# Performance work log

Measured on AMD Instinct MI355X. Metric: run time of the kernel, lower is better.

Reference implementation:

```python
import jax, jax.numpy as jnp
import numpy as np

N_USER, N_ITEM, D, K, E = 80000, 40000, 128, 10, 2000000

def _mlp(x, w1, b1, w2, b2, w3, b3):
    # MLP from source: linear->tanh->linear->tanh->linear->L2 normalize (eval mode, dropout off)
    x = jnp.tanh(x @ w1 + b1)
    x = jnp.tanh(x @ w2 + b2)
    x = x @ w3 + b3
    return x / jnp.maximum(jnp.linalg.norm(x, axis=-1, keepdims=True), 1e-12)

def setup_inputs() -> dict:
    key = jax.random.key(0)
    ks = jax.random.split(key, 24)
    s = 0.05
    inp = {
        'uemb_s': jax.random.normal(ks[0], (N_USER, D), jnp.float32),
        'iemb_s': jax.random.normal(ks[1], (N_ITEM, D), jnp.float32),
        'uemb_t': jax.random.normal(ks[2], (N_USER, D), jnp.float32),
        'u_emb_sp': jax.random.normal(ks[3], (N_USER, D), jnp.float32),
        'edge_user': jax.random.randint(ks[4], (E,), 0, N_USER, jnp.int32),
        'edge_item': jax.random.randint(ks[5], (E,), 0, N_ITEM, jnp.int32),
        # meta nets
        'Wu': jax.random.normal(ks[6], (4 * D, D), jnp.float32) * s,
        'bu': jnp.zeros((D,), jnp.float32),
        'Wi': jax.random.normal(ks[7], (2 * D, D), jnp.float32) * s,
        'bi': jnp.zeros((D,), jnp.float32),
        # mlp1: D -> D*K -> D//2 -> D*K
        'm1w1': jax.random.normal(ks[8], (D, D * K), jnp.float32) * s,
        'm1b1': jnp.zeros((D * K,), jnp.float32),
        'm1w2': jax.random.normal(ks[9], (D * K, D // 2), jnp.float32) * s,
        'm1b2': jnp.zeros((D // 2,), jnp.float32),
        'm1w3': jax.random.normal(ks[10], (D // 2, D * K), jnp.float32) * s,
        'm1b3': jnp.zeros((D * K,), jnp.float32),
        # mlp2: D -> D*K -> D//2 -> D*K
        'm2w1': jax.random.normal(ks[11], (D, D * K), jnp.float32) * s,
        'm2b1': jnp.zeros((D * K,), jnp.float32),
        'm2w2': jax.random.normal(ks[12], (D * K, D // 2), jnp.float32) * s,
        'm2b2': jnp.zeros((D // 2,), jnp.float32),
        'm2w3': jax.random.normal(ks[13], (D // 2, D * K), jnp.float32) * s,
        'm2b3': jnp.zeros((D * K,), jnp.float32),
    }
    return inp

def reference(uemb_s, iemb_s, uemb_t, u_emb_sp, edge_user, edge_item,
              Wu, bu, Wi, bi,
              m1w1, m1b1, m1w2, m1b2, m1w3, m1b3,
              m2w1, m2b1, m2w2, m2b2, m2w3, m2b3):
    # spmm with all-ones values == gather + segment_sum over the bipartite edge list
    neighbors_u = jax.ops.segment_sum(iemb_s[edge_item], edge_user, num_segments=N_USER)  # [U, D]
    tmp_embu = jax.lax.stop_gradient(
        jnp.concatenate([uemb_s, uemb_t, u_emb_sp, neighbors_u], axis=1)) @ Wu + bu       # [U, D]
    neighbors_i = jax.ops.segment_sum(((uemb_s + u_emb_sp) * 0.5)[edge_user], edge_item,
                                      num_segments=N_ITEM)                               # [I, D]
    tmp_embi = jax.lax.stop_gradient(
        jnp.concatenate([iemb_s, neighbors_i], axis=1)) @ Wi + bi                         # [I, D]
    metau = _mlp(tmp_embu, m1w1, m1b1, m1w2, m1b2, m1w3, m1b3).reshape(-1, D, K)          # [U, D, K]
    metai = _mlp(tmp_embi, m2w1, m2b1, m2w2, m2b2, m2w3, m2b3).reshape(-1, K, D)          # [I, K, D]
    meta_biasu = jnp.mean(metau, axis=0)  # [D, K]
    meta_biasi = jnp.mean(metai, axis=0)  # [K, D]
    low_weightu = jax.nn.softmax(metau + meta_biasu, axis=1)
    low_weighti = jax.nn.softmax(metai + meta_biasi, axis=1)
    return (low_weightu, low_weighti)
```

## Files before the change

### kernel.cpp

```cpp
#include <hip/hip_runtime.h>
#include <hip/hip_bf16.h>

#define D_ 128
#define DK_ 1280
#define K_ 10

typedef __attribute__((ext_vector_type(8))) short bh8;
typedef __attribute__((ext_vector_type(4))) short bh4;
typedef __attribute__((ext_vector_type(4))) float f32x4;

__device__ __forceinline__ short f2b(float f) {
    unsigned u = __builtin_bit_cast(unsigned, f);
    u += 0x7fffu + ((u >> 16) & 1u);
    return (short)(u >> 16);
}
__device__ __forceinline__ float b2f(short s) {
    unsigned u = ((unsigned)(unsigned short)s) << 16;
    return __builtin_bit_cast(float, u);
}
__device__ __forceinline__ float tanh_fast(float x) {
    float e = __expf(2.f * x);
    return 1.f - __fdividef(2.f, e + 1.f);
}
__device__ __forceinline__ f32x4 mfma16(bh8 a, bh8 b, f32x4 c) {
    return __builtin_amdgcn_mfma_f32_16x16x32_bf16(a, b, c, 0, 0, 0);
}

__device__ __forceinline__ int blk_excl_scan(int v, int t) {
    __shared__ int wp[4];
    int lane = t & 63, w = t >> 6;
    int s = v;
    for (int o = 1; o < 64; o <<= 1) {
        int pv = __shfl_up(s, o);
        if (lane >= o) s += pv;
    }
    if (lane == 63) wp[w] = s;
    __syncthreads();
    if (t == 0) {
        int a = 0;
#pragma unroll
        for (int k = 0; k < 4; ++k) { int x = wp[k]; wp[k] = a; a += x; }
    }
    __syncthreads();
    int r = s - v + wp[w];
    __syncthreads();
    return r;
}

__global__ __launch_bounds__(256) void cvt_all(
    const float* __restrict__ us, const float* __restrict__ ut,
    const float* __restrict__ usp, const float* __restrict__ is_,
    short* __restrict__ usb, short* __restrict__ utb,
    short* __restrict__ uspb, short* __restrict__ uavg, short* __restrict__ isb,
    int n4u, int n4i)
{
    int i = blockIdx.x * 256 + threadIdx.x;
    if (i < n4u) {
        float4 a = ((const float4*)us)[i];
        float4 b = ((const float4*)ut)[i];
        float4 c = ((const float4*)usp)[i];
        bh4 sa, sb, sc, sv;
        sa[0] = f2b(a.x); sa[1] = f2b(a.y); sa[2] = f2b(a.z); sa[3] = f2b(a.w);
        sb[0] = f2b(b.x); sb[1] = f2b(b.y); sb[2] = f2b(b.z); sb[3] = f2b(b.w);
        sc[0] = f2b(c.x); sc[1] = f2b(c.y); sc[2] = f2b(c.z); sc[3] = f2b(c.w);
        sv[0] = f2b(0.5f * (a.x + c.x)); sv[1] = f2b(0.5f * (a.y + c.y));
        sv[2] = f2b(0.5f * (a.z + c.z)); sv[3] = f2b(0.5f * (a.w + c.w));
        ((bh4*)usb)[i] = sa; ((bh4*)utb)[i] = sb;
        ((bh4*)uspb)[i] = sc; ((bh4*)uavg)[i] = sv;
    } else if (i < n4u + n4i) {
        int j = i - n4u;
        float4 v = ((const float4*)is_)[j];
        bh4 s;
        s[0] = f2b(v.x); s[1] = f2b(v.y); s[2] = f2b(v.z); s[3] = f2b(v.w);
        ((bh4*)isb)[j] = s;
    }
}

struct PackArgs {
    const float* W[8];
    short* o[8];
    int K[8];
    int N[8];
};
__global__ __launch_bounds__(256) void pack_all(PackArgs pa)
{
    int seg = blockIdx.y;
    int K = pa.K[seg], N = pa.N[seg];
    int total = K * N;
    int o = blockIdx.x * 256 + threadIdx.x;
    if (o >= total) return;
    const float* W = pa.W[seg];
    short* out = pa.o[seg];
    int j    = o & 7;
    int lane = (o >> 3) & 63;
    int rest = o >> 9;
    int KK = K >> 5;
    int kk = rest % KK;
    int tile = rest / KK;
    int k = kk * 32 + (lane >> 4) * 8 + j;
    int n = tile * 16 + (lane & 15);
    out[o] = f2b(W[(size_t)k * N + n]);
}

__global__ __launch_bounds__(256) void bhist_kernel(
    const int* __restrict__ eu, const int* __restrict__ ei,
    int* __restrict__ bcu, int* __restrict__ bci,
    int E, int shu, int shi, int nbu, int nbi)
{
    __shared__ int hu[160], hi[160];
    int t = threadIdx.x;
    int base = blockIdx.x * 4096;
    if (t < 160) { hu[t] = 0; hi[t] = 0; }
    __syncthreads();
    int n = min(4096, E - base);
#pragma unroll 4
    for (int k = 0; k < 16; ++k) {
        int idx = k * 256 + t;
        if (idx < n) {
            atomicAdd(&hu[eu[base + idx] >> shu], 1);
            atomicAdd(&hi[ei[base + idx] >> shi], 1);
        }
    }
    __syncthreads();
    if (t < nbu && hu[t]) atomicAdd(&bcu[t], hu[t]);
    if (t < nbi && hi[t]) atomicAdd(&bci[t], hi[t]);
}

__global__ __launch_bounds__(256) void binit_kernel(
    const int* __restrict__ bcu, int* __restrict__ gcu, int* __restrict__ bbu, int nbu,
    const int* __restrict__ bci, int* __restrict__ gci, int* __restrict__ bbi, int nbi,
    int E)
{
    int t = threadIdx.x;
    {
        int v = (t < nbu) ? bcu[t] : 0;
        int ex = blk_excl_scan(v, t);
        if (t < nbu) { gcu[t] = ex; bbu[t] = ex; }
        if (t == 0) bbu[nbu] = E;
    }
    __syncthreads();
    {
        int v = (t < nbi) ? bci[t] : 0;
        int ex = blk_excl_scan(v, t);
        if (t < nbi) { gci[t] = ex; bbi[t] = ex; }
        if (t == 0) bbi[nbi] = E;
    }
}

__global__ __launch_bounds__(256) void partition_kernel(
    const int* __restrict__ eu, const int* __restrict__ ei,
    int* __restrict__ gcu, int* __restrict__ gci,
    uint2* __restrict__ ebu, uint2* __restrict__ ebi,
    int E, int shu, int shi, int nbu, int nbi)
{
    __shared__ int hu[160], hi[160];
    int t = threadIdx.x;
    int base = blockIdx.x * 4096;
    if (t < 160) { hu[t] = 0; hi[t] = 0; }
    __syncthreads();
    int n = min(4096, E - base);
    int us[16], is_[16];
#pragma unroll 4
    for (int k = 0; k < 16; ++k) {
        int idx = k * 256 + t;
        if (idx < n) {
            us[k] = eu[base + idx];
            is_[k] = ei[base + idx];
            atomicAdd(&hu[us[k] >> shu], 1);
            atomicAdd(&hi[is_[k] >> shi], 1);
        } else us[k] = -1;
    }
    __syncthreads();
    if (t < nbu) { int c = hu[t]; hu[t] = c ? atomicAdd(&gcu[t], c) : 0; }
    if (t < nbi) { int c = hi[t]; hi[t] = c ? atomicAdd(&gci[t], c) : 0; }
    __syncthreads();
#pragma unroll 4
    for (int k = 0; k < 16; ++k) {
        if (us[k] >= 0) {
            int p1 = atomicAdd(&hu[us[k] >> shu], 1);
            ebu[p1] = make_uint2((unsigned)us[k], (unsigned)is_[k]);
            int p2 = atomicAdd(&hi[is_[k] >> shi], 1);
            ebi[p2] = make_uint2((unsigned)is_[k], (unsigned)us[k]);
        }
    }
}

__global__ __launch_bounds__(256) void fill2_kernel(
    const uint2* __restrict__ ebuf, const int* __restrict__ bbase,
    int* __restrict__ off, int* __restrict__ end_, int* __restrict__ adj,
    int span_sh, int nrows)
{
    __shared__ int lcnt[512];
    __shared__ int lcur[512];
    int t = threadIdx.x;
    int b = blockIdx.x;
    int rbase = b << span_sh;
    int span = min(1 << span_sh, nrows - rbase);
    int regbeg = bbase[b], regend = bbase[b + 1];
    for (int j = t; j < span; j += 256) lcnt[j] = 0;
    __syncthreads();
    for (int e = regbeg + t; e < regend; e += 256)
        atomicAdd(&lcnt[ebuf[e].x - rbase], 1);
    __syncthreads();
    int c0 = (2 * t < span) ? lcnt[2 * t] : 0;
    int c1 = (2 * t + 1 < span) ? lcnt[2 * t + 1] : 0;
    int ex = blk_excl_scan(c0 + c1, t);
    if (2 * t < span) {
        int beg = regbeg + ex;
        off[rbase + 2 * t] = beg;
        end_[rbase + 2 * t] = beg + c0;
        lcur[2 * t] = beg;
    }
    if (2 * t + 1 < span) {
        int beg = regbeg + ex + c0;
        off[rbase + 2 * t + 1] = beg;
        end_[rbase + 2 * t + 1] = beg + c1;
        lcur[2 * t + 1] = beg;
    }
    __syncthreads();
    for (int e = regbeg + t; e < regend; e += 256) {
        uint2 p = ebuf[e];
        int slot = atomicAdd(&lcur[p.x - rbase], 1);
        adj[slot] = (int)p.y;
    }
}

__global__ __launch_bounds__(256) void gather_kernel(
    const short* __restrict__ emb,
    const int* __restrict__ off, const int* __restrict__ end_,
    const int* __restrict__ adj, short* __restrict__ out, int M)
{
    int wid = (blockIdx.x * 256 + threadIdx.x) >> 6;
    if (wid >= M) return;
    int lane = threadIdx.x & 63;
    int beg = off[wid], end = end_[wid];
    float ax = 0.f, ay = 0.f;
    int j = beg;
    for (; j + 3 < end; j += 4) {
        unsigned a = *(const unsigned*)(emb + (size_t)adj[j]     * D_ + lane * 2);
        unsigned b = *(const unsigned*)(emb + (size_t)adj[j + 1] * D_ + lane * 2);
        unsigned c = *(const unsigned*)(emb + (size_t)adj[j + 2] * D_ + lane * 2);
        unsigned d = *(const unsigned*)(emb + (size_t)adj[j + 3] * D_ + lane * 2);
        ax += b2f((short)(a & 0xffff)) + b2f((short)(b & 0xffff))
            + b2f((short)(c & 0xffff)) + b2f((short)(d & 0xffff));
        ay += b2f((short)(a >> 16)) + b2f((short)(b >> 16))
            + b2f((short)(c >> 16)) + b2f((short)(d >> 16));
    }
    for (; j < end; ++j) {
        unsigned a = *(const unsigned*)(emb + (size_t)adj[j] * D_ + lane * 2);
        ax += b2f((short)(a & 0xffff));
        ay += b2f((short)(a >> 16));
    }
    unsigned o = ((unsigned)(unsigned short)f2b(ay) << 16) | (unsigned short)(unsigned)f2b(ax);
    *(unsigned*)(out + (size_t)wid * D_ + lane * 2) = o;
}

template<int KCAT, int NARR>
__global__ __launch_bounds__(256, 3) void fused_mlp(
    const short* __restrict__ A0, const short* __restrict__ A1,
    const short* __restrict__ A2, const short* __restrict__ A3,
    const short* __restrict__ Wg, const float* __restrict__ bg,
    const short* __restrict__ W1p, const float* __restrict__ b1,
    const short* __restrict__ W2p, const float* __restrict__ b2,
    const short* __restrict__ W3p, const float* __restrict__ b3,
    short* __restrict__ Ybf, float* __restrict__ bsum)
{
    __shared__ char pool[47104];
    __shared__ float wred[4][16];
    __shared__ float nrms[16];

    short* x2 = (short*)pool;
    short* xc = (short*)(pool + 4096);
    short* h1 = (short*)(pool + 4096);
    short* h2 = (short*)(pool + 45056);
    short* yb = (short*)pool;

    const int t = threadIdx.x;
    const int l = t & 63;
    const int w = t >> 6;
    const int lr = l & 15;
    const int lg = l >> 4;
    const size_t rb0 = (size_t)blockIdx.x * 16;

    constexpr int CH_ROW = KCAT / 8;
    constexpr int NITER = (16 * CH_ROW) / 256;
#pragma unroll
    for (int j = 0; j < NITER; ++j) {
        int idx = j * 256 + t;
        int row = idx / CH_ROW;
        int slot = idx % CH_ROW;
        int a = slot >> 4, cs = slot & 15;
        const short* src = (NARR == 4) ? (a == 0 ? A0 : a == 1 ? A1 : a == 2 ? A2 : A3)
                                       : (a == 0 ? A0 : A1);
        bh8 v = *(const bh8*)(src + (rb0 + row) * D_ + cs * 8);
        int sl2 = slot ^ (row & 7);
        *(bh8*)(xc + row * KCAT + sl2 * 8) = v;
    }
    __syncthreads();

    {
        constexpr int KK_G = KCAT / 32;
        f32x4 accA0 = {0,0,0,0}, accB0 = accA0, accA1 = accA0, accB1 = accA0;
#pragma unroll 4
        for (int kk = 0; kk < KK_G; ++kk) {
            int slot = kk * 4 + lg;
            bh8 af = *(const bh8*)(xc + lr * KCAT + (slot ^ (lr & 7)) * 8);
            bh8 b0 = *(const bh8*)(Wg + (((size_t)(2 * w)     * KK_G + kk) * 64 + l) * 8);
            bh8 b1v = *(const bh8*)(Wg + (((size_t)(2 * w + 1) * KK_G + kk) * 64 + l) * 8);
            if (kk & 1) { accB0 = mfma16(af, b0, accB0); accB1 = mfma16(af, b1v, accB1); }
            else        { accA0 = mfma16(af, b0, accA0); accA1 = mfma16(af, b1v, accA1); }
        }
#pragma unroll
        for (int r = 0; r < 4; ++r) {
            int row = lg * 4 + r;
            int c0 = (2 * w) * 16 + lr;
            int c1 = c0 + 16;
            x2[row * 128 + (((c0 >> 3) ^ (row & 7)) * 8) + (l & 7)] = f2b(accA0[r] + accB0[r] + bg[c0]);
            x2[row * 128 + (((c1 >> 3) ^ (row & 7)) * 8) + (l & 7)] = f2b(accA1[r] + accB1[r] + bg[c1]);
        }
    }
    __syncthreads();

    {
        bh8 a1f[4];
#pragma unroll
        for (int kk = 0; kk < 4; ++kk) {
            int slot = kk * 4 + lg;
            a1f[kk] = *(const bh8*)(x2 + lr * 128 + (slot ^ (lr & 7)) * 8);
        }
#pragma unroll 2
        for (int tile = w * 20; tile < w * 20 + 20; ++tile) {
            float bv = b1[tile * 16 + lr];
            f32x4 acc = {bv, bv, bv, bv};
#pragma unroll
            for (int kk = 0; kk < 4; ++kk) {
                bh8 bf_ = *(const bh8*)(W1p + (((size_t)tile * 4 + kk) * 64 + l) * 8);
                acc = mfma16(a1f[kk], bf_, acc);
            }
#pragma unroll
            for (int r = 0; r < 4; ++r) {
                int row = lg * 4 + r;
                int col = tile * 16 + lr;
                h1[row * 1280 + (((col >> 3) ^ (row & 7)) * 8) + (l & 7)] = f2b(tanh_fast(acc[r]));
            }
        }
    }
    __syncthreads();

    {
        float bv = b2[w * 16 + lr];
        f32x4 accA = {bv, bv, bv, bv}, accB = {0,0,0,0};
#pragma unroll 4
        for (int kk = 0; kk < 40; ++kk) {
            int slot = kk * 4 + lg;
            bh8 af = *(const bh8*)(h1 + lr * 1280 + (slot ^ (lr & 7)) * 8);
            bh8 bf_ = *(const bh8*)(W2p + (((size_t)w * 40 + kk) * 64 + l) * 8);
            if (kk & 1) accB = mfma16(af, bf_, accB);
            else        accA = mfma16(af, bf_, accA);
        }
#pragma unroll
        for (int r = 0; r < 4; ++r) {
            int row = lg * 4 + r;
            int col = w * 16 + lr;
            h2[row * 64 + (((col >> 3) ^ (row & 7)) * 8) + (l & 7)] = f2b(tanh_fast(accA[r] + accB[r]));
        }
    }
    __syncthreads();

    {
        bh8 a3[2];
#pragma unroll
        for (int kk = 0; kk < 2; ++kk) {
            int slot = kk * 4 + lg;
            a3[kk] = *(const bh8*)(h2 + lr * 64 + (slot ^ (lr & 7)) * 8);
        }
        float ssq[4] = {0.f, 0.f, 0.f, 0.f};
#pragma unroll 2
        for (int tile = w * 20; tile < w * 20 + 20; ++tile) {
            float bv = b3[tile * 16 + lr];
            f32x4 acc = {bv, bv, bv, bv};
            bh8 b0 = *(const bh8*)(W3p + (((size_t)tile * 2 + 0) * 64 + l) * 8);
            bh8 b1v = *(const bh8*)(W3p + (((size_t)tile * 2 + 1) * 64 + l) * 8);
            acc = mfma16(a3[0], b0, acc);
            acc = mfma16(a3[1], b1v, acc);
            bh4 pk;
#pragma unroll
            for (int r = 0; r < 4; ++r) {
                ssq[r] = fmaf(acc[r], acc[r], ssq[r]);
                pk[r] = f2b(acc[r]);
            }
            *(bh4*)(yb + tile * 260 + l * 4) = pk;
        }
#pragma unroll
        for (int off = 1; off < 16; off <<= 1) {
#pragma unroll
            for (int r = 0; r < 4; ++r) ssq[r] += __shfl_xor(ssq[r], off);
        }
        if (lr == 0) {
#pragma unroll
            for (int r = 0; r < 4; ++r) wred[w][lg * 4 + r] = ssq[r];
        }
    }
    __syncthreads();
    if (t < 16) {
        float s = wred[0][t] + wred[1][t] + wred[2][t] + wred[3][t];
        nrms[t] = 1.f / fmaxf(sqrtf(s), 1e-12f);
    }
    __syncthreads();

    {
        float csum[5] = {0.f, 0.f, 0.f, 0.f, 0.f};
        for (int row = 0; row < 16; ++row) {
            float nv = nrms[row];
            int lph = (row >> 2) << 4;
            int r = row & 3;
#pragma unroll
            for (int ch = 0; ch < 5; ++ch) {
                int c = ch * 256 + t;
                int tile = c >> 4;
                int lanep = lph | (c & 15);
                float v = b2f(yb[tile * 260 + lanep * 4 + r]) * nv;
                Ybf[(rb0 + row) * DK_ + c] = f2b(v);
                csum[ch] += v;
            }
        }
#pragma unroll
        for (int ch = 0; ch < 5; ++ch) atomicAdd(&bsum[ch * 256 + t], csum[ch]);
    }
}

__global__ __launch_bounds__(64) void softmax_u_kernel(
    const short* __restrict__ Ab, const float* __restrict__ bsum, float invM,
    float* __restrict__ Out)
{
    __shared__ float rowb[DK_];
    int u = blockIdx.x;
    int t = threadIdx.x;
    size_t base = (size_t)u * DK_;
    for (int i = t; i < DK_ / 2; i += 64) {
        unsigned a = ((const unsigned*)(Ab + base))[i];
        float2 bv = ((const float2*)bsum)[i];
        rowb[2 * i]     = b2f((short)(a & 0xffff)) + bv.x * invM;
        rowb[2 * i + 1] = b2f((short)(a >> 16))    + bv.y * invM;
    }
    __syncthreads();
#pragma unroll 1
    for (int k = 0; k < K_; ++k) {
        float v0 = rowb[t * K_ + k];
        float v1 = rowb[(t + 64) * K_ + k];
        float m = fmaxf(v0, v1);
        for (int off = 32; off; off >>= 1) m = fmaxf(m, __shfl_xor(m, off));
        float e0 = expf(v0 - m), e1 = expf(v1 - m);
        float s = e0 + e1;
        for (int off = 32; off; off >>= 1) s += __shfl_xor(s, off);
        float rs = 1.f / s;
        rowb[t * K_ + k] = e0 * rs;
        rowb[(t + 64) * K_ + k] = e1 * rs;
    }
    __syncthreads();
    for (int i = t; i < DK_; i += 64) Out[base + i] = rowb[i];
}

__global__ __launch_bounds__(128) void softmax_i_kernel(
    const short* __restrict__ Ab, const float* __restrict__ bsum, float invM,
    float* __restrict__ Out)
{
    int it = blockIdx.x;
    int t = threadIdx.x;
    size_t base = (size_t)it * DK_;
    float v[K_];
    float m = -1e30f;
#pragma unroll
    for (int k = 0; k < K_; ++k) {
        v[k] = b2f(Ab[base + k * D_ + t]) + bsum[k * D_ + t] * invM;
        m = fmaxf(m, v[k]);
    }
    float s = 0.f;
#pragma unroll
    for (int k = 0; k < K_; ++k) { v[k] = expf(v[k] - m); s += v[k]; }
    float rs = 1.f / s;
#pragma unroll
    for (int k = 0; k < K_; ++k) Out[base + k * D_ + t] = v[k] * rs;
}

extern "C" void kernel_launch(void* const* d_in, const int* in_sizes, int n_in,
                              void* d_out, int out_size, void* d_ws, size_t ws_size,
                              hipStream_t stream)
{
    const float* uemb_s   = (const float*)d_in[0];
    const float* iemb_s   = (const float*)d_in[1];
    const float* uemb_t   = (const float*)d_in[2];
    const float* u_emb_sp = (const float*)d_in[3];
    const int*   eu       = (const int*)d_in[4];
    const int*   ei       = (const int*)d_in[5];
    const float* Wu  = (const float*)d_in[6];
    const float* bu  = (const float*)d_in[7];
    const float* Wi  = (const float*)d_in[8];
    const float* bi  = (const float*)d_in[9];
    const float* m1w1 = (const float*)d_in[10];
    const float* m1b1 = (const float*)d_in[11];
    const float* m1w2 = (const float*)d_in[12];
    const float* m1b2 = (const float*)d_in[13];
    const float* m1w3 = (const float*)d_in[14];
    const float* m1b3 = (const float*)d_in[15];
    const float* m2w1 = (const float*)d_in[16];
    const float* m2b1 = (const float*)d_in[17];
    const float* m2w2 = (const float*)d_in[18];
    const float* m2b2 = (const float*)d_in[19];
    const float* m2w3 = (const float*)d_in[20];
    const float* m2b3 = (const float*)d_in[21];

    const int U = in_sizes[0] / D_;
    const int I = in_sizes[1] / D_;
    const int E = in_sizes[4];

    const int SHU = 9, SHI = 8;
    const int NBU = (U + 511) >> 9;
    const int NBI = (I + 255) >> 8;

    char* p = (char*)d_ws;
    auto alloc = [&](size_t bytes) { char* r = p; p += (bytes + 255) & ~(size_t)255; return r; };

    short* usb  = (short*)alloc((size_t)U * D_ * 2);
    short* utb  = (short*)alloc((size_t)U * D_ * 2);
    short* uspb = (short*)alloc((size_t)U * D_ * 2);
    short* uavg = (short*)alloc((size_t)U * D_ * 2);
    short* isb  = (short*)alloc((size_t)I * D_ * 2);
    short* nub  = (short*)alloc((size_t)U * D_ * 2);
    short* nib  = (short*)alloc((size_t)I * D_ * 2);
    short* ybu  = (short*)alloc((size_t)U * DK_ * 2);
    short* ybi  = (short*)alloc((size_t)I * DK_ * 2);
    short* WgU  = (short*)alloc(512 * 128 * 2);
    short* WgI  = (short*)alloc(256 * 128 * 2);
    short* W1U  = (short*)alloc(128 * 1280 * 2);
    short* W2U  = (short*)alloc(1280 * 64 * 2);
    short* W3U  = (short*)alloc(64 * 1280 * 2);
    short* W1I  = (short*)alloc(128 * 1280 * 2);
    short* W2I  = (short*)alloc(1280 * 64 * 2);
    short* W3I  = (short*)alloc(64 * 1280 * 2);
    float* bsu  = (float*)alloc(DK_ * 4);
    float* bsi  = (float*)alloc(DK_ * 4);
    int* bcnt   = (int*)alloc(320 * 4);
    int* bcnt_u = bcnt;
    int* bcnt_i = bcnt + 160;
    int* gcur_u = (int*)alloc(160 * 4);
    int* gcur_i = (int*)alloc(160 * 4);
    int* bbase_u = (int*)alloc(161 * 4);
    int* bbase_i = (int*)alloc(161 * 4);
    int* off_u  = (int*)alloc((size_t)U * 4);
    int* end_u  = (int*)alloc((size_t)U * 4);
    int* off_i  = (int*)alloc((size_t)I * 4);
    int* end_i  = (int*)alloc((size_t)I * 4);
    uint2* ebu  = (uint2*)alloc((size_t)E * 8);
    uint2* ebi  = (uint2*)alloc((size_t)E * 8);
    int* adj_u  = (int*)alloc((size_t)E * 4);
    int* adj_i  = (int*)alloc((size_t)E * 4);

    float* outu = (float*)d_out;
    float* outi = outu + (size_t)U * DK_;

    hipMemsetAsync(bcnt, 0, 320 * 4, stream);
    hipMemsetAsync(bsu, 0, DK_ * 4, stream);
    hipMemsetAsync(bsi, 0, DK_ * 4, stream);

    int n4u = U * D_ / 4, n4i = I * D_ / 4;
    cvt_all<<<(n4u + n4i + 255) / 256, 256, 0, stream>>>(
        uemb_s, uemb_t, u_emb_sp, iemb_s, usb, utb, uspb, uavg, isb, n4u, n4i);

    PackArgs pa;
    pa.W[0] = Wu;   pa.o[0] = WgU; pa.K[0] = 512;  pa.N[0] = 128;
    pa.W[1] = Wi;   pa.o[1] = WgI; pa.K[1] = 256;  pa.N[1] = 128;
    pa.W[2] = m1w1; pa.o[2] = W1U; pa.K[2] = 128;  pa.N[2] = 1280;
    pa.W[3] = m1w2; pa.o[3] = W2U; pa.K[3] = 1280; pa.N[3] = 64;
    pa.W[4] = m1w3; pa.o[4] = W3U; pa.K[4] = 64;   pa.N[4] = 1280;
    pa.W[5] = m2w1; pa.o[5] = W1I; pa.K[5] = 128;  pa.N[5] = 1280;
    pa.W[6] = m2w2; pa.o[6] = W2I; pa.K[6] = 1280; pa.N[6] = 64;
    pa.W[7] = m2w3; pa.o[7] = W3I; pa.K[7] = 64;   pa.N[7] = 1280;
    pack_all<<<dim3(640, 8), 256, 0, stream>>>(pa);

    int pb = (E + 4095) / 4096;
    bhist_kernel<<<pb, 256, 0, stream>>>(eu, ei, bcnt_u, bcnt_i, E, SHU, SHI, NBU, NBI);
    binit_kernel<<<1, 256, 0, stream>>>(bcnt_u, gcur_u, bbase_u, NBU,
                                        bcnt_i, gcur_i, bbase_i, NBI, E);
    partition_kernel<<<pb, 256, 0, stream>>>(eu, ei, gcur_u, gcur_i, ebu, ebi,
                                             E, SHU, SHI, NBU, NBI);
    fill2_kernel<<<NBU, 256, 0, stream>>>(ebu, bbase_u, off_u, end_u, adj_u, SHU, U);
    fill2_kernel<<<NBI, 256, 0, stream>>>(ebi, bbase_i, off_i, end_i, adj_i, SHI, I);

    gather_kernel<<<(U + 3) / 4, 256, 0, stream>>>(isb,  off_u, end_u, adj_u, nub, U);
    gather_kernel<<<(I + 3) / 4, 256, 0, stream>>>(uavg, off_i, end_i, adj_i, nib, I);

    fused_mlp<512, 4><<<U / 16, 256, 0, stream>>>(
        usb, utb, uspb, nub, WgU, bu, W1U, m1b1, W2U, m1b2, W3U, m1b3, ybu, bsu);
    fused_mlp<256, 2><<<I / 16, 256, 0, stream>>>(
        isb, nib, nullptr, nullptr, WgI, bi, W1I, m2b1, W2I, m2b2, W3I, m2b3, ybi, bsi);

    softmax_u_kernel<<<U, 64, 0, stream>>>(ybu, bsu, 1.0f / (float)U, outu);
    softmax_i_kernel<<<I, 128, 0, stream>>>(ybi, bsi, 1.0f / (float)I, outi);
}
```

Before: 931.2 us.

## Merge user/item kernel pairs into single launches and replace bias atomics with partials

Merges the paired user and item launches of fill, gather, fused MLP and softmax into single kernels that branch on block index. This cuts launch count and lets the smaller item work fill the tail of the user grids. The per-block atomicAdd into the mean-bias accumulator becomes per-block partial sums, reduced by a new finalize_bias kernel. The item softmax now runs with 64 threads per row, each handling two columns with vectorized loads and stores. The three memsets are collapsed into one. In exchange, the MLP template constants become runtime values, which may weaken compiler unrolling and addressing, and a partial-sum buffer adds extra memory traffic.

```diff
diff --git a/kernel.cpp b/kernel.cpp
--- a/kernel.cpp
+++ b/kernel.cpp
@@ -185,15 +185,26 @@
     }
 }
 
-__global__ __launch_bounds__(256) void fill2_kernel(
-    const uint2* __restrict__ ebuf, const int* __restrict__ bbase,
-    int* __restrict__ off, int* __restrict__ end_, int* __restrict__ adj,
-    int span_sh, int nrows)
+__global__ __launch_bounds__(256) void fill2_all(
+    const uint2* __restrict__ ebu, const int* __restrict__ bbu,
+    int* __restrict__ off_u, int* __restrict__ end_u, int* __restrict__ adj_u,
+    int NBU, int U,
+    const uint2* __restrict__ ebi, const int* __restrict__ bbi,
+    int* __restrict__ off_i, int* __restrict__ end_i, int* __restrict__ adj_i, int I)
 {
     __shared__ int lcnt[512];
     __shared__ int lcur[512];
+    bool isU = (int)blockIdx.x < NBU;
+    const uint2* ebuf = isU ? ebu : ebi;
+    const int* bbase  = isU ? bbu : bbi;
+    int* off  = isU ? off_u : off_i;
+    int* end_ = isU ? end_u : end_i;
+    int* adj  = isU ? adj_u : adj_i;
+    int span_sh = isU ? 9 : 8;
+    int nrows = isU ? U : I;
+    int b = isU ? blockIdx.x : blockIdx.x - NBU;
+
     int t = threadIdx.x;
-    int b = blockIdx.x;
     int rbase = b << span_sh;
     int span = min(1 << span_sh, nrows - rbase);
     int regbeg = bbase[b], regend = bbase[b + 1];
@@ -225,45 +236,54 @@
     }
 }
 
-__global__ __launch_bounds__(256) void gather_kernel(
-    const short* __restrict__ emb,
-    const int* __restrict__ off, const int* __restrict__ end_,
-    const int* __restrict__ adj, short* __restrict__ out, int M)
-{
-    int wid = (blockIdx.x * 256 + threadIdx.x) >> 6;
-    if (wid >= M) return;
+__global__ __launch_bounds__(256) void gather_all(
+    const short* __restrict__ embU, const short* __restrict__ embI,
+    const int* __restrict__ off_u, const int* __restrict__ end_u, const int* __restrict__ adj_u,
+    const int* __restrict__ off_i, const int* __restrict__ end_i, const int* __restrict__ adj_i,
+    short* __restrict__ nub, short* __restrict__ nib, int U, int I)
+{
+    int gw = (blockIdx.x * 256 + threadIdx.x) >> 6;
     int lane = threadIdx.x & 63;
-    int beg = off[wid], end = end_[wid];
+    const short* emb; const int *offp, *endp, *adjp; short* outp; int row;
+    if (gw < U)          { emb = embU; offp = off_u; endp = end_u; adjp = adj_u; outp = nub; row = gw; }
+    else if (gw < U + I) { emb = embI; offp = off_i; endp = end_i; adjp = adj_i; outp = nib; row = gw - U; }
+    else return;
+
+    int beg = offp[row], end = endp[row];
     float ax = 0.f, ay = 0.f;
     int j = beg;
     for (; j + 3 < end; j += 4) {
-        unsigned a = *(const unsigned*)(emb + (size_t)adj[j]     * D_ + lane * 2);
-        unsigned b = *(const unsigned*)(emb + (size_t)adj[j + 1] * D_ + lane * 2);
-        unsigned c = *(const unsigned*)(emb + (size_t)adj[j + 2] * D_ + lane * 2);
-        unsigned d = *(const unsigned*)(emb + (size_t)adj[j + 3] * D_ + lane * 2);
+        unsigned a = *(const unsigned*)(emb + (size_t)adjp[j]     * D_ + lane * 2);
+        unsigned b = *(const unsigned*)(emb + (size_t)adjp[j + 1] * D_ + lane * 2);
+        unsigned c = *(const unsigned*)(emb + (size_t)adjp[j + 2] * D_ + lane * 2);
+        unsigned d = *(const unsigned*)(emb + (size_t)adjp[j + 3] * D_ + lane * 2);
         ax += b2f((short)(a & 0xffff)) + b2f((short)(b & 0xffff))
             + b2f((short)(c & 0xffff)) + b2f((short)(d & 0xffff));
         ay += b2f((short)(a >> 16)) + b2f((short)(b >> 16))
             + b2f((short)(c >> 16)) + b2f((short)(d >> 16));
     }
     for (; j < end; ++j) {
-        unsigned a = *(const unsigned*)(emb + (size_t)adj[j] * D_ + lane * 2);
+        unsigned a = *(const unsigned*)(emb + (size_t)adjp[j] * D_ + lane * 2);
         ax += b2f((short)(a & 0xffff));
         ay += b2f((short)(a >> 16));
     }
     unsigned o = ((unsigned)(unsigned short)f2b(ay) << 16) | (unsigned short)(unsigned)f2b(ax);
-    *(unsigned*)(out + (size_t)wid * D_ + lane * 2) = o;
-}
-
-template<int KCAT, int NARR>
-__global__ __launch_bounds__(256, 3) void fused_mlp(
-    const short* __restrict__ A0, const short* __restrict__ A1,
-    const short* __restrict__ A2, const short* __restrict__ A3,
-    const short* __restrict__ Wg, const float* __restrict__ bg,
-    const short* __restrict__ W1p, const float* __restrict__ b1,
-    const short* __restrict__ W2p, const float* __restrict__ b2,
-    const short* __restrict__ W3p, const float* __restrict__ b3,
-    short* __restrict__ Ybf, float* __restrict__ bsum)
+    *(unsigned*)(outp + (size_t)row * D_ + lane * 2) = o;
+}
+
+struct MlpArgs {
+    const short *uA0, *uA1, *uA2, *uA3;
+    const short *iA0, *iA1;
+    const short *uWg, *uW1, *uW2, *uW3;
+    const short *iWg, *iW1, *iW2, *iW3;
+    const float *ubg, *ub1, *ub2, *ub3;
+    const float *ibg, *ib1, *ib2, *ib3;
+    short *uY, *iY;
+    float *uPart, *iPart;
+    int UB;
+};
+
+__global__ __launch_bounds__(256, 3) void fused_mlp_all(MlpArgs P)
 {
     __shared__ char pool[47104];
     __shared__ float wred[4][16];
@@ -280,33 +300,44 @@
     const int w = t >> 6;
     const int lr = l & 15;
     const int lg = l >> 4;
-    const size_t rb0 = (size_t)blockIdx.x * 16;
-
-    constexpr int CH_ROW = KCAT / 8;
-    constexpr int NITER = (16 * CH_ROW) / 256;
-#pragma unroll
-    for (int j = 0; j < NITER; ++j) {
-        int idx = j * 256 + t;
-        int row = idx / CH_ROW;
-        int slot = idx % CH_ROW;
+
+    const bool isU = (int)blockIdx.x < P.UB;
+    const int bid = isU ? (int)blockIdx.x : (int)blockIdx.x - P.UB;
+    const size_t rb0 = (size_t)bid * 16;
+    const int CHSH = isU ? 6 : 5;
+    const int KKG  = isU ? 16 : 8;
+    const short* Wg = isU ? P.uWg : P.iWg;
+    const short* W1 = isU ? P.uW1 : P.iW1;
+    const short* W2 = isU ? P.uW2 : P.iW2;
+    const short* W3 = isU ? P.uW3 : P.iW3;
+    const float* bg = isU ? P.ubg : P.ibg;
+    const float* b1 = isU ? P.ub1 : P.ib1;
+    const float* b2 = isU ? P.ub2 : P.ib2;
+    const float* b3 = isU ? P.ub3 : P.ib3;
+    short* Ybf = isU ? P.uY : P.iY;
+    float* part = (isU ? P.uPart : P.iPart) + (size_t)bid * DK_;
+
+    const int CH_ROW = 1 << CHSH;
+    for (int idx = t; idx < (16 << CHSH); idx += 256) {
+        int row = idx >> CHSH;
+        int slot = idx & (CH_ROW - 1);
         int a = slot >> 4, cs = slot & 15;
-        const short* src = (NARR == 4) ? (a == 0 ? A0 : a == 1 ? A1 : a == 2 ? A2 : A3)
-                                       : (a == 0 ? A0 : A1);
+        const short* src = isU ? (a == 0 ? P.uA0 : a == 1 ? P.uA1 : a == 2 ? P.uA2 : P.uA3)
+                               : (a == 0 ? P.iA0 : P.iA1);
         bh8 v = *(const bh8*)(src + (rb0 + row) * D_ + cs * 8);
         int sl2 = slot ^ (row & 7);
-        *(bh8*)(xc + row * KCAT + sl2 * 8) = v;
+        *(bh8*)(xc + (row << (CHSH + 3)) + sl2 * 8) = v;
     }
     __syncthreads();
 
     {
-        constexpr int KK_G = KCAT / 32;
         f32x4 accA0 = {0,0,0,0}, accB0 = accA0, accA1 = accA0, accB1 = accA0;
 #pragma unroll 4
-        for (int kk = 0; kk < KK_G; ++kk) {
+        for (int kk = 0; kk < KKG; ++kk) {
             int slot = kk * 4 + lg;
-            bh8 af = *(const bh8*)(xc + lr * KCAT + (slot ^ (lr & 7)) * 8);
-            bh8 b0 = *(const bh8*)(Wg + (((size_t)(2 * w)     * KK_G + kk) * 64 + l) * 8);
-            bh8 b1v = *(const bh8*)(Wg + (((size_t)(2 * w + 1) * KK_G + kk) * 64 + l) * 8);
+            bh8 af = *(const bh8*)(xc + (lr << (CHSH + 3)) + ((slot ^ (lr & 7)) * 8));
+            bh8 b0 = *(const bh8*)(Wg + (((size_t)(2 * w) * KKG + kk) * 64 + l) * 8);
+            bh8 b1v = *(const bh8*)(Wg + (((size_t)(2 * w + 1) * KKG + kk) * 64 + l) * 8);
             if (kk & 1) { accB0 = mfma16(af, b0, accB0); accB1 = mfma16(af, b1v, accB1); }
             else        { accA0 = mfma16(af, b0, accA0); accA1 = mfma16(af, b1v, accA1); }
         }
@@ -334,7 +365,7 @@
             f32x4 acc = {bv, bv, bv, bv};
 #pragma unroll
             for (int kk = 0; kk < 4; ++kk) {
-                bh8 bf_ = *(const bh8*)(W1p + (((size_t)tile * 4 + kk) * 64 + l) * 8);
+                bh8 bf_ = *(const bh8*)(W1 + (((size_t)tile * 4 + kk) * 64 + l) * 8);
                 acc = mfma16(a1f[kk], bf_, acc);
             }
 #pragma unroll
@@ -354,7 +385,7 @@
         for (int kk = 0; kk < 40; ++kk) {
             int slot = kk * 4 + lg;
             bh8 af = *(const bh8*)(h1 + lr * 1280 + (slot ^ (lr & 7)) * 8);
-            bh8 bf_ = *(const bh8*)(W2p + (((size_t)w * 40 + kk) * 64 + l) * 8);
+            bh8 bf_ = *(const bh8*)(W2 + (((size_t)w * 40 + kk) * 64 + l) * 8);
             if (kk & 1) accB = mfma16(af, bf_, accB);
             else        accA = mfma16(af, bf_, accA);
         }
@@ -379,8 +410,8 @@
         for (int tile = w * 20; tile < w * 20 + 20; ++tile) {
             float bv = b3[tile * 16 + lr];
             f32x4 acc = {bv, bv, bv, bv};
-            bh8 b0 = *(const bh8*)(W3p + (((size_t)tile * 2 + 0) * 64 + l) * 8);
-            bh8 b1v = *(const bh8*)(W3p + (((size_t)tile * 2 + 1) * 64 + l) * 8);
+            bh8 b0 = *(const bh8*)(W3 + (((size_t)tile * 2 + 0) * 64 + l) * 8);
+            bh8 b1v = *(const bh8*)(W3 + (((size_t)tile * 2 + 1) * 64 + l) * 8);
             acc = mfma16(a3[0], b0, acc);
             acc = mfma16(a3[1], b1v, acc);
             bh4 pk;
@@ -425,62 +456,91 @@
             }
         }
 #pragma unroll
-        for (int ch = 0; ch < 5; ++ch) atomicAdd(&bsum[ch * 256 + t], csum[ch]);
-    }
-}
-
-__global__ __launch_bounds__(64) void softmax_u_kernel(
-    const short* __restrict__ Ab, const float* __restrict__ bsum, float invM,
-    float* __restrict__ Out)
+        for (int ch = 0; ch < 5; ++ch) part[ch * 256 + t] = csum[ch];
+    }
+}
+
+__global__ __launch_bounds__(256) void finalize_bias(
+    const float* __restrict__ partU, const float* __restrict__ partI,
+    float* __restrict__ bsu, float* __restrict__ bsi, int NU, int NI)
+{
+    int c = blockIdx.x * 256 + threadIdx.x;
+    int z = blockIdx.z;
+    const float* part = z ? partI : partU;
+    float* dst = z ? bsi : bsu;
+    int M = z ? NI : NU;
+    int chunk = (M + gridDim.y - 1) / gridDim.y;
+    int r0 = blockIdx.y * chunk;
+    int r1 = min(M, r0 + chunk);
+    if (r0 >= r1) return;
+    float s = 0.f;
+    for (int r = r0; r < r1; ++r) s += part[(size_t)r * DK_ + c];
+    atomicAdd(&dst[c], s);
+}
+
+__global__ __launch_bounds__(64) void softmax_all(
+    const short* __restrict__ Yu, const short* __restrict__ Yi,
+    const float* __restrict__ bsu, const float* __restrict__ bsi,
+    float invU, float invI,
+    float* __restrict__ outu, float* __restrict__ outi, int U, int I)
 {
     __shared__ float rowb[DK_];
-    int u = blockIdx.x;
+    int b = blockIdx.x;
     int t = threadIdx.x;
-    size_t base = (size_t)u * DK_;
-    for (int i = t; i < DK_ / 2; i += 64) {
-        unsigned a = ((const unsigned*)(Ab + base))[i];
-        float2 bv = ((const float2*)bsum)[i];
-        rowb[2 * i]     = b2f((short)(a & 0xffff)) + bv.x * invM;
-        rowb[2 * i + 1] = b2f((short)(a >> 16))    + bv.y * invM;
-    }
-    __syncthreads();
+    if (b < U) {
+        size_t base = (size_t)b * DK_;
+        for (int i = t; i < DK_ / 4; i += 64) {
+            uint2 a = ((const uint2*)(Yu + base))[i];
+            float4 bv = ((const float4*)bsu)[i];
+            rowb[4 * i + 0] = b2f((short)(a.x & 0xffff)) + bv.x * invU;
+            rowb[4 * i + 1] = b2f((short)(a.x >> 16))    + bv.y * invU;
+            rowb[4 * i + 2] = b2f((short)(a.y & 0xffff)) + bv.z * invU;
+            rowb[4 * i + 3] = b2f((short)(a.y >> 16))    + bv.w * invU;
+        }
+        __syncthreads();
 #pragma unroll 1
-    for (int k = 0; k < K_; ++k) {
-        float v0 = rowb[t * K_ + k];
-        float v1 = rowb[(t + 64) * K_ + k];
-        float m = fmaxf(v0, v1);
-        for (int off = 32; off; off >>= 1) m = fmaxf(m, __shfl_xor(m, off));
-        float e0 = expf(v0 - m), e1 = expf(v1 - m);
-        float s = e0 + e1;
-        for (int off = 32; off; off >>= 1) s += __shfl_xor(s, off);
-        float rs = 1.f / s;
-        rowb[t * K_ + k] = e0 * rs;
-        rowb[(t + 64) * K_ + k] = e1 * rs;
-    }
-    __syncthreads();
-    for (int i = t; i < DK_; i += 64) Out[base + i] = rowb[i];
-}
-
-__global__ __launch_bounds__(128) void softmax_i_kernel(
-    const short* __restrict__ Ab, const float* __restrict__ bsum, float invM,
-    float* __restrict__ Out)
-{
-    int it = blockIdx.x;
-    int t = threadIdx.x;
-    size_t base = (size_t)it * DK_;
-    float v[K_];
-    float m = -1e30f;
-#pragma unroll
-    for (int k = 0; k < K_; ++k) {
-        v[k] = b2f(Ab[base + k * D_ + t]) + bsum[k * D_ + t] * invM;
-        m = fmaxf(m, v[k]);
-    }
-    float s = 0.f;
-#pragma unroll
-    for (int k = 0; k < K_; ++k) { v[k] = expf(v[k] - m); s += v[k]; }
-    float rs = 1.f / s;
-#pragma unroll
-    for (int k = 0; k < K_; ++k) Out[base + k * D_ + t] = v[k] * rs;
+        for (int k = 0; k < K_; ++k) {
+            float v0 = rowb[t * K_ + k];
+            float v1 = rowb[(t + 64) * K_ + k];
+            float m = fmaxf(v0, v1);
+            for (int off = 32; off; off >>= 1) m = fmaxf(m, __shfl_xor(m, off));
+            float e0 = expf(v0 - m), e1 = expf(v1 - m);
+            float s = e0 + e1;
+            for (int off = 32; off; off >>= 1) s += __shfl_xor(s, off);
+            float rs = 1.f / s;
+            rowb[t * K_ + k] = e0 * rs;
+            rowb[(t + 64) * K_ + k] = e1 * rs;
+        }
+        __syncthreads();
+        for (int i = t; i < DK_ / 4; i += 64)
+            ((float4*)(outu + base))[i] = ((const float4*)rowb)[i];
+    } else {
+        int it = b - U;
+        if (it >= I) return;
+        size_t base = (size_t)it * DK_;
+        float v0[K_], v1[K_];
+        float m0 = -1e30f, m1 = -1e30f;
+#pragma unroll
+        for (int k = 0; k < K_; ++k) {
+            unsigned a = *(const unsigned*)(Yi + base + k * D_ + 2 * t);
+            float2 bv = ((const float2*)(bsi + k * D_))[t];
+            v0[k] = b2f((short)(a & 0xffff)) + bv.x * invI;
+            v1[k] = b2f((short)(a >> 16))    + bv.y * invI;
+            m0 = fmaxf(m0, v0[k]); m1 = fmaxf(m1, v1[k]);
+        }
+        float s0 = 0.f, s1 = 0.f;
+#pragma unroll
+        for (int k = 0; k < K_; ++k) {
+            v0[k] = expf(v0[k] - m0); s0 += v0[k];
+            v1[k] = expf(v1[k] - m1); s1 += v1[k];
+        }
+        float r0 = 1.f / s0, r1 = 1.f / s1;
+#pragma unroll
+        for (int k = 0; k < K_; ++k) {
+            float2 o; o.x = v0[k] * r0; o.y = v1[k] * r1;
+            ((float2*)(outi + base + k * D_))[t] = o;
+        }
+    }
 }
 
 extern "C" void kernel_launch(void* const* d_in, const int* in_sizes, int n_in,
@@ -517,6 +577,7 @@
     const int SHU = 9, SHI = 8;
     const int NBU = (U + 511) >> 9;
     const int NBI = (I + 255) >> 8;
+    const int UB = U / 16, IB = I / 16;
 
     char* p = (char*)d_ws;
     auto alloc = [&](size_t bytes) { char* r = p; p += (bytes + 255) & ~(size_t)255; return r; };
@@ -530,6 +591,8 @@
     short* nib  = (short*)alloc((size_t)I * D_ * 2);
     short* ybu  = (short*)alloc((size_t)U * DK_ * 2);
     short* ybi  = (short*)alloc((size_t)I * DK_ * 2);
+    float* partU = (float*)alloc((size_t)UB * DK_ * 4);
+    float* partI = (float*)alloc((size_t)IB * DK_ * 4);
     short* WgU  = (short*)alloc(512 * 128 * 2);
     short* WgI  = (short*)alloc(256 * 128 * 2);
     short* W1U  = (short*)alloc(128 * 1280 * 2);
@@ -538,11 +601,11 @@
     short* W1I  = (short*)alloc(128 * 1280 * 2);
     short* W2I  = (short*)alloc(1280 * 64 * 2);
     short* W3I  = (short*)alloc(64 * 1280 * 2);
-    float* bsu  = (float*)alloc(DK_ * 4);
-    float* bsi  = (float*)alloc(DK_ * 4);
-    int* bcnt   = (int*)alloc(320 * 4);
-    int* bcnt_u = bcnt;
-    int* bcnt_i = bcnt + 160;
+    int*   zbuf = (int*)alloc((320 + 2 * DK_) * 4);
+    int* bcnt_u = zbuf;
+    int* bcnt_i = zbuf + 160;
+    float* bsu  = (float*)(zbuf + 320);
+    float* bsi  = bsu + DK_;
     int* gcur_u = (int*)alloc(160 * 4);
     int* gcur_i = (int*)alloc(160 * 4);
     int* bbase_u = (int*)alloc(161 * 4);
@@ -559,9 +622,7 @@
     float* outu = (float*)d_out;
     float* outi = outu + (size_t)U * DK_;
 
-    hipMemsetAsync(bcnt, 0, 320 * 4, stream);
-    hipMemsetAsync(bsu, 0, DK_ * 4, stream);
-    hipMemsetAsync(bsi, 0, DK_ * 4, stream);
+    hipMemsetAsync(zbuf, 0, (320 + 2 * DK_) * 4, stream);
 
     int n4u = U * D_ / 4, n4i = I * D_ / 4;
     cvt_all<<<(n4u + n4i + 255) / 256, 256, 0, stream>>>(
@@ -584,17 +645,26 @@
                                         bcnt_i, gcur_i, bbase_i, NBI, E);
     partition_kernel<<<pb, 256, 0, stream>>>(eu, ei, gcur_u, gcur_i, ebu, ebi,
                                              E, SHU, SHI, NBU, NBI);
-    fill2_kernel<<<NBU, 256, 0, stream>>>(ebu, bbase_u, off_u, end_u, adj_u, SHU, U);
-    fill2_kernel<<<NBI, 256, 0, stream>>>(ebi, bbase_i, off_i, end_i, adj_i, SHI, I);
-
-    gather_kernel<<<(U + 3) / 4, 256, 0, stream>>>(isb,  off_u, end_u, adj_u, nub, U);
-    gather_kernel<<<(I + 3) / 4, 256, 0, stream>>>(uavg, off_i, end_i, adj_i, nib, I);
-
-    fused_mlp<512, 4><<<U / 16, 256, 0, stream>>>(
-        usb, utb, uspb, nub, WgU, bu, W1U, m1b1, W2U, m1b2, W3U, m1b3, ybu, bsu);
-    fused_mlp<256, 2><<<I / 16, 256, 0, stream>>>(
-        isb, nib, nullptr, nullptr, WgI, bi, W1I, m2b1, W2I, m2b2, W3I, m2b3, ybi, bsi);
-
-    softmax_u_kernel<<<U, 64, 0, stream>>>(ybu, bsu, 1.0f / (float)U, outu);
-    softmax_i_kernel<<<I, 128, 0, stream>>>(ybi, bsi, 1.0f / (float)I, outi);
-}
+    fill2_all<<<NBU + NBI, 256, 0, stream>>>(ebu, bbase_u, off_u, end_u, adj_u, NBU, U,
+                                             ebi, bbase_i, off_i, end_i, adj_i, I);
+
+    gather_all<<<(U + I + 3) / 4, 256, 0, stream>>>(
+        isb, uavg, off_u, end_u, adj_u, off_i, end_i, adj_i, nub, nib, U, I);
+
+    MlpArgs ma;
+    ma.uA0 = usb; ma.uA1 = utb; ma.uA2 = uspb; ma.uA3 = nub;
+    ma.iA0 = isb; ma.iA1 = nib;
+    ma.uWg = WgU; ma.uW1 = W1U; ma.uW2 = W2U; ma.uW3 = W3U;
+    ma.iWg = WgI; ma.iW1 = W1I; ma.iW2 = W2I; ma.iW3 = W3I;
+    ma.ubg = bu; ma.ub1 = m1b1; ma.ub2 = m1b2; ma.ub3 = m1b3;
+    ma.ibg = bi; ma.ib1 = m2b1; ma.ib2 = m2b2; ma.ib3 = m2b3;
+    ma.uY = ybu; ma.iY = ybi;
+    ma.uPart = partU; ma.iPart = partI;
+    ma.UB = UB;
+    fused_mlp_all<<<UB + IB, 256, 0, stream>>>(ma);
+
+    finalize_bias<<<dim3(5, 40, 2), 256, 0, stream>>>(partU, partI, bsu, bsi, UB, IB);
+
+    softmax_all<<<U + I, 64, 0, stream>>>(ybu, ybi, bsu, bsi,
+                                          1.0f / (float)U, 1.0f / (float)I, outu, outi, U, I);
+}
```

New measurement: 880.4 us. -5.5%, faster.
